# Kernel tuning notes

Hardware: AMD Instinct MI355X
Metric: run time of the kernel (lower is better)

The kernel has to match this reference:

```python
import jax, jax.numpy as jnp
import numpy as np

NUM_HEADS = 16
HEAD_DIM = 64
HIDDEN = NUM_HEADS * HEAD_DIM  # 1024
Q_DIM = 512
KV_DIM = 256


def setup_inputs() -> dict:
    key = jax.random.key(0)
    k1, k2, k3, k4, k5, k6 = jax.random.split(key, 6)
    B, I, J = 64, 128, 512  # num_assets, num_latents, window_size
    q = jax.random.normal(k1, (B, I, Q_DIM), dtype=jnp.float32)
    kv = jax.random.normal(k2, (B, J, KV_DIM), dtype=jnp.float32)
    # Linear weights stored as (in, out); fan-in scaled init
    Wq = jax.random.normal(k3, (Q_DIM, HIDDEN), dtype=jnp.float32) / np.sqrt(Q_DIM)
    Wkv = jax.random.normal(k4, (KV_DIM, 2 * HIDDEN), dtype=jnp.float32) / np.sqrt(KV_DIM)
    Wo = jax.random.normal(k5, (HIDDEN, Q_DIM), dtype=jnp.float32) / np.sqrt(HIDDEN)
    bo = jax.random.normal(k6, (Q_DIM,), dtype=jnp.float32) * 0.01
    return {"q": q, "kv": kv, "Wq": Wq, "Wkv": Wkv, "Wo": Wo, "bo": bo}


def reference(q, kv, Wq, Wkv, Wo, bo):
    B, I, _ = q.shape
    J = kv.shape[1]
    scale = HEAD_DIM ** -0.5
    query = q @ Wq                              # (B, I, HIDDEN)
    k, v = jnp.split(kv @ Wkv, 2, axis=-1)      # each (B, J, HIDDEN)
    qh = query.reshape(B, I, NUM_HEADS, HEAD_DIM).transpose(0, 2, 1, 3)  # bhid
    kh = k.reshape(B, J, NUM_HEADS, HEAD_DIM).transpose(0, 2, 1, 3)      # bhjd
    vh = v.reshape(B, J, NUM_HEADS, HEAD_DIM).transpose(0, 2, 1, 3)      # bhjd
    scores = jnp.einsum('bhid,bhjd->bhij', qh, kh) * scale
    attn = jax.nn.softmax(scores, axis=-1)
    out = jnp.einsum('bhij,bhjd->bhid', attn, vh)
    out = out.transpose(0, 2, 1, 3).reshape(B, I, HIDDEN)
    return out @ Wo + bo
```

## Files before the change

kernel.cpp:

```cpp
#include <hip/hip_runtime.h>
#include <stdint.h>

typedef unsigned short ushort_t;
typedef __attribute__((ext_vector_type(8))) short short8;
typedef __attribute__((ext_vector_type(4))) float floatx4;
typedef __attribute__((ext_vector_type(4))) float floatv4;
typedef __attribute__((ext_vector_type(4))) unsigned short ushortv4;


__device__ __forceinline__ ushort_t f2bf(float x) {
    union { float f; unsigned u; } v; v.f = x;
    unsigned r = v.u + 0x7fffu + ((v.u >> 16) & 1u);
    return (ushort_t)(r >> 16);
}

__device__ __forceinline__ void gl_lds16(const ushort_t* g, ushort_t* l) {
    __builtin_amdgcn_global_load_lds(
        (const __attribute__((address_space(1))) void*)g,
        (__attribute__((address_space(3))) void*)l, 16, 0, 0);
}

__global__ __launch_bounds__(256) void prep_kernel(
    const float* __restrict__ q, const float* __restrict__ kv,
    const float* __restrict__ Wq, const float* __restrict__ Wkv,
    const float* __restrict__ Wo,
    ushort_t* __restrict__ qA, ushort_t* __restrict__ kvA,
    ushort_t* __restrict__ WqT, ushort_t* __restrict__ WkvT,
    ushort_t* __restrict__ WoT)
{
    __shared__ ushort_t tileS[64 * 68];
    const int bid = blockIdx.x;
    const int tid = threadIdx.x;
    if (bid < 6144) {
        const float* src = (bid < 2048) ? q : kv;
        ushort_t* dst    = (bid < 2048) ? qA : kvA;
        size_t t = (size_t)(bid < 2048 ? bid : bid - 2048) * 256 + tid;
        const float* s = src + t * 8;
        floatv4 v0 = *(const floatv4*)s;
        floatv4 v1 = *(const floatv4*)(s + 4);
        short8 o;
        o[0] = (short)f2bf(v0[0]); o[1] = (short)f2bf(v0[1]);
        o[2] = (short)f2bf(v0[2]); o[3] = (short)f2bf(v0[3]);
        o[4] = (short)f2bf(v1[0]); o[5] = (short)f2bf(v1[1]);
        o[6] = (short)f2bf(v1[2]); o[7] = (short)f2bf(v1[3]);
        *(short8*)&dst[t * 8] = o;
        return;
    }
    const float* src; ushort_t* dst; int K, N, kt, nt; float scale = 1.0f;
    if (bid < 6272)      { int tl = bid - 6144; src = Wq;  dst = WqT;  K = 512;  N = 1024; kt = tl >> 4; nt = tl & 15; scale = 0.125f; }
    else if (bid < 6400) { int tl = bid - 6272; src = Wkv; dst = WkvT; K = 256;  N = 2048; kt = tl >> 5; nt = tl & 31; }
    else                 { int tl = bid - 6400; src = Wo;  dst = WoT;  K = 1024; N = 512;  kt = tl >> 3; nt = tl & 7;  }
#pragma unroll
    for (int t = 0; t < 4; t++) {
        int e = t * 256 + tid;
        int row = e >> 4, c4 = e & 15;
        floatv4 v = *(const floatv4*)&src[(size_t)(kt * 64 + row) * N + nt * 64 + c4 * 4];
        ushortv4 o;
        o[0] = f2bf(v[0] * scale); o[1] = f2bf(v[1] * scale);
        o[2] = f2bf(v[2] * scale); o[3] = f2bf(v[3] * scale);
        *(ushortv4*)&tileS[row * 68 + c4 * 4] = o;
    }
    __syncthreads();
#pragma unroll
    for (int t = 0; t < 4; t++) {
        int e = t * 256 + tid;
        int orow = e >> 4, c4 = e & 15;
        ushortv4 o;
#pragma unroll
        for (int e2 = 0; e2 < 4; e2++) o[e2] = tileS[(c4 * 4 + e2) * 68 + orow];
        *(ushortv4*)&dst[(size_t)(nt * 64 + orow) * K + kt * 64 + c4 * 4] = o;
    }
}

__global__ __launch_bounds__(256, 4) void gemm_bt_kernel(
    const ushort_t* __restrict__ A, const ushort_t* __restrict__ Bt,
    int M, int N, int K,
    float* __restrict__ out_f, const float* __restrict__ bias)
{
    __shared__ ushort_t smem[8192];
    ushort_t* sA = smem;
    ushort_t* sB = smem + 4096;

    const int bid  = blockIdx.x;
    const int xcd  = bid & 7;
    const int slot = bid >> 3;
    const int by   = xcd * 16 + (slot & 15);
    const int bx   = slot >> 4;

    const int tid  = threadIdx.x;
    const int lane = tid & 63;
    const int w    = tid >> 6;
    const int quad = lane >> 4;
    const int l15  = lane & 15;
    const int wr   = w >> 1, wc = w & 1;
    const int m0 = by * 64;
    const int n0 = bx * 64;

    const int rsub = lane >> 3;
    const int c8   = lane & 7;

    floatx4 acc[2][2];
#pragma unroll
    for (int i = 0; i < 2; i++)
#pragma unroll
        for (int j = 0; j < 2; j++) acc[i][j] = (floatx4){0.f, 0.f, 0.f, 0.f};

    for (int k0 = 0; k0 < K; k0 += 64) {
        __syncthreads();
#pragma unroll
        for (int t = 0; t < 2; t++) {
            int rg = w * 16 + t * 8;
            gl_lds16(&A[(size_t)(m0 + rg + rsub) * K + k0 + c8 * 8], &sA[rg * 64]);
            gl_lds16(&Bt[(size_t)(n0 + rg + rsub) * K + k0 + c8 * 8], &sB[rg * 64]);
        }
        __syncthreads();
#pragma unroll
        for (int ks = 0; ks < 64; ks += 32) {
            short8 af[2], bf[2];
#pragma unroll
            for (int i = 0; i < 2; i++)
                af[i] = *(const short8*)&sA[(wr * 32 + i * 16 + l15) * 64 + ks + quad * 8];
#pragma unroll
            for (int j = 0; j < 2; j++)
                bf[j] = *(const short8*)&sB[(wc * 32 + j * 16 + l15) * 64 + ks + quad * 8];
#pragma unroll
            for (int i = 0; i < 2; i++)
#pragma unroll
                for (int j = 0; j < 2; j++)
                    acc[i][j] = __builtin_amdgcn_mfma_f32_16x16x32_bf16(
                        af[i], bf[j], acc[i][j], 0, 0, 0);
        }
    }

#pragma unroll
    for (int i = 0; i < 2; i++)
#pragma unroll
        for (int j = 0; j < 2; j++)
#pragma unroll
            for (int r = 0; r < 4; r++) {
                int grow = m0 + wr * 32 + i * 16 + quad * 4 + r;
                int gcol = n0 + wc * 32 + j * 16 + l15;
                out_f[(size_t)grow * N + gcol] = acc[i][j][r] + bias[gcol];
            }
}

__global__ __launch_bounds__(512, 4) void fattn_kernel(
    const ushort_t* __restrict__ QA,
    const ushort_t* __restrict__ WQ,
    const ushort_t* __restrict__ KV,
    const ushort_t* __restrict__ W,
    ushort_t* __restrict__ O)
{
    __shared__ ushort_t smem[34816];
    ushort_t* sKV = smem;
    ushort_t* sKc = smem + 16384;
    ushort_t* sVt = smem + 20992;
    ushort_t* sP  = smem + 25600;
    ushort_t* sQ  = smem;
    ushort_t* sW  = smem + 16384;

    const int bid  = blockIdx.x;
    const int xcd  = bid & 7;
    const int slot = bid >> 3;
    const int b = xcd * 8 + (slot & 7);
    const int h = slot >> 3;

    const int tid  = threadIdx.x;
    const int lane = tid & 63, w = tid >> 6;
    const int quad = lane >> 4, l15 = lane & 15;
    const int swz  = (l15 & 7) << 3;

    ushort_t* sp = &sP[w * 1152];

    const int rq = lane >> 4;
    const int gq = l15 * 8;
    const int rh = lane >> 5;
    const int gk = (lane & 31) * 8;

    const ushort_t* qb = &QA[(size_t)b * 128 * 512];
    const ushort_t* wq = &WQ[(size_t)h * 64 * 512];
    floatx4 qacc[4];
#pragma unroll
    for (int nt = 0; nt < 4; nt++) qacc[nt] = (floatx4){0.f, 0.f, 0.f, 0.f};

    for (int kc = 0; kc < 4; kc++) {
        if (kc) __syncthreads();
#pragma unroll
        for (int t = 0; t < 4; t++) {
            int rb = w * 16 + t * 4;
            int srow = rb + rq;
            int scol = kc * 128 + (gq ^ ((srow & 7) << 3));
            gl_lds16(&qb[(size_t)srow * 512 + scol], &sQ[rb * 128]);
        }
#pragma unroll
        for (int t = 0; t < 2; t++) {
            int rb = w * 8 + t * 4;
            int srow = rb + rq;
            int scol = kc * 128 + (gq ^ ((srow & 7) << 3));
            gl_lds16(&wq[(size_t)srow * 512 + scol], &sW[rb * 128]);
        }
        __syncthreads();
#pragma unroll
        for (int ks = 0; ks < 4; ks++) {
            short8 af = *(const short8*)&sQ[(w * 16 + l15) * 128 + ((ks * 32 + quad * 8) ^ swz)];
#pragma unroll
            for (int nt = 0; nt < 4; nt++) {
                short8 bfr = *(const short8*)&sW[(nt * 16 + l15) * 128 + ((ks * 32 + quad * 8) ^ swz)];
                qacc[nt] = __builtin_amdgcn_mfma_f32_16x16x32_bf16(af, bfr, qacc[nt], 0, 0, 0);
            }
        }
    }
    __syncthreads();

    const ushort_t* kvb = &KV[(size_t)b * 512 * 256];
#define STAGE_KV(CH)                                                          \
    {                                                                         \
        _Pragma("unroll")                                                     \
        for (int t = 0; t < 4; t++) {                                         \
            int rloc = 8 * w + 2 * t;          \
            int srow = rloc + rh;                                             \
            int scol = gk ^ ((srow & 7) << 3);                                \
            gl_lds16(&kvb[(size_t)((CH) * 64 + srow) * 256 + scol],           \
                     &sKV[rloc * 256]);                                       \
        }                                                                     \
    }
    STAGE_KV(0);

#pragma unroll
    for (int nt = 0; nt < 4; nt++)
#pragma unroll
        for (int r = 0; r < 4; r++)
            sp[(quad * 4 + r) * 72 + nt * 16 + l15] = f2bf(qacc[nt][r]);
    short8 aq0 = *(const short8*)&sp[l15 * 72 + quad * 8];
    short8 aq1 = *(const short8*)&sp[l15 * 72 + 32 + quad * 8];

    short8 wf[8];
    {
        int n = w * 16 + l15;
        int grow = (n < 64) ? (h * 64 + n) : (1024 + h * 64 + (n - 64));
        const ushort_t* wp = &W[(size_t)grow * 256 + quad * 8];
#pragma unroll
        for (int ks = 0; ks < 8; ks++)
            wf[ks] = *(const short8*)(wp + ks * 32);
    }

    float lsum[4];
    floatx4 acc_o[4];
#pragma unroll
    for (int r = 0; r < 4; r++) lsum[r] = 0.f;
#pragma unroll
    for (int dt = 0; dt < 4; dt++) acc_o[dt] = (floatx4){0.f, 0.f, 0.f, 0.f};

    for (int ch = 0; ch < 8; ch++) {
        __syncthreads();

        floatx4 pacc[4];
#pragma unroll
        for (int jt = 0; jt < 4; jt++) pacc[jt] = (floatx4){0.f, 0.f, 0.f, 0.f};
#pragma unroll
        for (int ks = 0; ks < 8; ks++) {
            short8 af[4];
#pragma unroll
            for (int jt = 0; jt < 4; jt++)
                af[jt] = *(const short8*)&sKV[(jt * 16 + l15) * 256 + ((ks * 32 + quad * 8) ^ swz)];
#pragma unroll
            for (int jt = 0; jt < 4; jt++)
                pacc[jt] = __builtin_amdgcn_mfma_f32_16x16x32_bf16(
                    af[jt], wf[ks], pacc[jt], 0, 0, 0);
        }

        if (w < 4) {
            int d = w * 16 + l15;
#pragma unroll
            for (int jt = 0; jt < 4; jt++)
#pragma unroll
                for (int r = 0; r < 4; r++)
                    sKc[(jt * 16 + quad * 4 + r) * 72 + d] = f2bf(pacc[jt][r]);
        } else {
            int d = (w - 4) * 16 + l15;
#pragma unroll
            for (int jt = 0; jt < 4; jt++) {
                ushortv4 p;
#pragma unroll
                for (int r = 0; r < 4; r++) p[r] = f2bf(pacc[jt][r]);
                *(ushortv4*)&sVt[d * 72 + jt * 16 + quad * 4] = p;
            }
        }
        __syncthreads();

        if (ch < 7) STAGE_KV(ch + 1);

#pragma unroll
        for (int jt = 0; jt < 4; jt++) {
            const ushort_t* kp = &sKc[(jt * 16 + l15) * 72 + quad * 8];
            short8 bk0 = *(const short8*)kp;
            short8 bk1 = *(const short8*)(kp + 32);
            floatx4 a = (floatx4){0.f, 0.f, 0.f, 0.f};
            a = __builtin_amdgcn_mfma_f32_16x16x32_bf16(aq0, bk0, a, 0, 0, 0);
            a = __builtin_amdgcn_mfma_f32_16x16x32_bf16(aq1, bk1, a, 0, 0, 0);
            ushortv4 pk;
#pragma unroll
            for (int r = 0; r < 4; r++) {
                float p = __expf(a[r]);
                lsum[r] += p;
                pk[r] = f2bf(p);
            }
#pragma unroll
            for (int r = 0; r < 4; r++)
                sp[(quad * 4 + r) * 72 + jt * 16 + l15] = pk[r];
        }

#pragma unroll
        for (int kk = 0; kk < 2; kk++) {
            short8 ap = *(const short8*)&sp[l15 * 72 + kk * 32 + quad * 8];
#pragma unroll
            for (int dt = 0; dt < 4; dt++) {
                short8 bv = *(const short8*)&sVt[(dt * 16 + l15) * 72 + kk * 32 + quad * 8];
                acc_o[dt] = __builtin_amdgcn_mfma_f32_16x16x32_bf16(ap, bv, acc_o[dt], 0, 0, 0);
            }
        }
    }

#pragma unroll
    for (int r = 0; r < 4; r++) {
        float s = lsum[r];
#pragma unroll
        for (int off = 1; off < 16; off <<= 1) s += __shfl_xor(s, off);
        float inv = 1.0f / s;
        size_t rowo = (size_t)(b * 128 + w * 16 + quad * 4 + r) * 1024 + h * 64;
#pragma unroll
        for (int dt = 0; dt < 4; dt++)
            O[rowo + dt * 16 + l15] = f2bf(acc_o[dt][r] * inv);
    }
#undef STAGE_KV
}

extern "C" void kernel_launch(void* const* d_in, const int* in_sizes, int n_in,
                              void* d_out, int out_size, void* d_ws, size_t ws_size,
                              hipStream_t stream) {
    const float* q   = (const float*)d_in[0];
    const float* kv  = (const float*)d_in[1];
    const float* Wq  = (const float*)d_in[2];
    const float* Wkv = (const float*)d_in[3];
    const float* Wo  = (const float*)d_in[4];
    const float* bo  = (const float*)d_in[5];
    float* out = (float*)d_out;

    char* ws = (char*)d_ws;
    ushort_t* qA    = (ushort_t*)(ws + 0);
    ushort_t* kvA   = (ushort_t*)(ws + 8388608);
    ushort_t* WqT   = (ushort_t*)(ws + 25165824);
    ushort_t* WkvT  = (ushort_t*)(ws + 26214400);
    ushort_t* WoT   = (ushort_t*)(ws + 27262976);
    ushort_t* attnO = (ushort_t*)(ws + 45088768);

    hipLaunchKernelGGL(prep_kernel, dim3(6528), dim3(256), 0, stream,
                       q, kv, Wq, Wkv, Wo, qA, kvA, WqT, WkvT, WoT);

    hipLaunchKernelGGL(fattn_kernel, dim3(1024), dim3(512), 0, stream,
                       qA, WqT, kvA, WkvT, attnO);

    hipLaunchKernelGGL(gemm_bt_kernel, dim3(1024), dim3(256), 0, stream,
                       attnO, WoT, 8192, 512, 1024, out, bo);
}
```

Measured before the change: 202.4 us.

## Process two heads per attention block to share staged KV and Q tiles

The fused attention kernel now runs 1024-thread blocks covering two heads of the same batch item, halving the grid. Each block loads the KV chunk and the Q tile into LDS once and reuses them for both heads, with per-head K/V projection buffers. This cuts redundant global-to-LDS traffic for KV and Q. The cost is larger LDS use and bigger blocks, which may lower occupancy and make barriers more expensive.

```diff
diff --git a/kernel.cpp b/kernel.cpp
--- a/kernel.cpp
+++ b/kernel.cpp
@@ -144,33 +144,37 @@
             }
 }
 
-__global__ __launch_bounds__(512, 4) void fattn_kernel(
+__global__ __launch_bounds__(1024, 2) void fattn_kernel(
     const ushort_t* __restrict__ QA,
     const ushort_t* __restrict__ WQ,
     const ushort_t* __restrict__ KV,
     const ushort_t* __restrict__ W,
     ushort_t* __restrict__ O)
 {
-    __shared__ ushort_t smem[34816];
+    __shared__ ushort_t smem[53248];
     ushort_t* sKV = smem;
     ushort_t* sKc = smem + 16384;
-    ushort_t* sVt = smem + 20992;
-    ushort_t* sP  = smem + 25600;
+    ushort_t* sVt = smem + 25600;
+    ushort_t* sP  = smem + 34816;
     ushort_t* sQ  = smem;
     ushort_t* sW  = smem + 16384;
 
     const int bid  = blockIdx.x;
     const int xcd  = bid & 7;
     const int slot = bid >> 3;
-    const int b = xcd * 8 + (slot & 7);
-    const int h = slot >> 3;
+    const int b  = xcd * 8 + (slot & 7);
+    const int hp = slot >> 3;
 
     const int tid  = threadIdx.x;
     const int lane = tid & 63, w = tid >> 6;
+    const int hg   = w >> 3, wl = w & 7;
+    const int h    = hp * 2 + hg;
     const int quad = lane >> 4, l15 = lane & 15;
     const int swz  = (l15 & 7) << 3;
 
-    ushort_t* sp = &sP[w * 1152];
+    ushort_t* sp  = &sP[w * 1152];
+    ushort_t* sKc_g = &sKc[hg * 4608];
+    ushort_t* sVt_g = &sVt[hg * 4608];
 
     const int rq = lane >> 4;
     const int gq = l15 * 8;
@@ -178,34 +182,34 @@
     const int gk = (lane & 31) * 8;
 
     const ushort_t* qb = &QA[(size_t)b * 128 * 512];
-    const ushort_t* wq = &WQ[(size_t)h * 64 * 512];
+    const ushort_t* wqg = &WQ[(size_t)h * 64 * 512];
     floatx4 qacc[4];
 #pragma unroll
     for (int nt = 0; nt < 4; nt++) qacc[nt] = (floatx4){0.f, 0.f, 0.f, 0.f};
 
     for (int kc = 0; kc < 4; kc++) {
         if (kc) __syncthreads();
-#pragma unroll
-        for (int t = 0; t < 4; t++) {
-            int rb = w * 16 + t * 4;
-            int srow = rb + rq;
-            int scol = kc * 128 + (gq ^ ((srow & 7) << 3));
-            gl_lds16(&qb[(size_t)srow * 512 + scol], &sQ[rb * 128]);
-        }
 #pragma unroll
         for (int t = 0; t < 2; t++) {
             int rb = w * 8 + t * 4;
             int srow = rb + rq;
             int scol = kc * 128 + (gq ^ ((srow & 7) << 3));
-            gl_lds16(&wq[(size_t)srow * 512 + scol], &sW[rb * 128]);
+            gl_lds16(&qb[(size_t)srow * 512 + scol], &sQ[rb * 128]);
+        }
+#pragma unroll
+        for (int t = 0; t < 2; t++) {
+            int rb = wl * 8 + t * 4;
+            int srow = rb + rq;
+            int scol = kc * 128 + (gq ^ ((srow & 7) << 3));
+            gl_lds16(&wqg[(size_t)srow * 512 + scol], &sW[hg * 8192 + rb * 128]);
         }
         __syncthreads();
 #pragma unroll
         for (int ks = 0; ks < 4; ks++) {
-            short8 af = *(const short8*)&sQ[(w * 16 + l15) * 128 + ((ks * 32 + quad * 8) ^ swz)];
+            short8 af = *(const short8*)&sQ[(wl * 16 + l15) * 128 + ((ks * 32 + quad * 8) ^ swz)];
 #pragma unroll
             for (int nt = 0; nt < 4; nt++) {
-                short8 bfr = *(const short8*)&sW[(nt * 16 + l15) * 128 + ((ks * 32 + quad * 8) ^ swz)];
+                short8 bfr = *(const short8*)&sW[hg * 8192 + (nt * 16 + l15) * 128 + ((ks * 32 + quad * 8) ^ swz)];
                 qacc[nt] = __builtin_amdgcn_mfma_f32_16x16x32_bf16(af, bfr, qacc[nt], 0, 0, 0);
             }
         }
@@ -216,8 +220,8 @@
 #define STAGE_KV(CH)                                                          \
     {                                                                         \
         _Pragma("unroll")                                                     \
-        for (int t = 0; t < 4; t++) {                                         \
-            int rloc = 8 * w + 2 * t;          \
+        for (int t = 0; t < 2; t++) {                                         \
+            int rloc = 4 * w + 2 * t;          \
             int srow = rloc + rh;                                             \
             int scol = gk ^ ((srow & 7) << 3);                                \
             gl_lds16(&kvb[(size_t)((CH) * 64 + srow) * 256 + scol],           \
@@ -236,7 +240,7 @@
 
     short8 wf[8];
     {
-        int n = w * 16 + l15;
+        int n = wl * 16 + l15;
         int grow = (n < 64) ? (h * 64 + n) : (1024 + h * 64 + (n - 64));
         const ushort_t* wp = &W[(size_t)grow * 256 + quad * 8];
 #pragma unroll
@@ -269,21 +273,21 @@
                     af[jt], wf[ks], pacc[jt], 0, 0, 0);
         }
 
-        if (w < 4) {
-            int d = w * 16 + l15;
+        if (wl < 4) {
+            int d = wl * 16 + l15;
 #pragma unroll
             for (int jt = 0; jt < 4; jt++)
 #pragma unroll
                 for (int r = 0; r < 4; r++)
-                    sKc[(jt * 16 + quad * 4 + r) * 72 + d] = f2bf(pacc[jt][r]);
+                    sKc_g[(jt * 16 + quad * 4 + r) * 72 + d] = f2bf(pacc[jt][r]);
         } else {
-            int d = (w - 4) * 16 + l15;
+            int d = (wl - 4) * 16 + l15;
 #pragma unroll
             for (int jt = 0; jt < 4; jt++) {
                 ushortv4 p;
 #pragma unroll
                 for (int r = 0; r < 4; r++) p[r] = f2bf(pacc[jt][r]);
-                *(ushortv4*)&sVt[d * 72 + jt * 16 + quad * 4] = p;
+                *(ushortv4*)&sVt_g[d * 72 + jt * 16 + quad * 4] = p;
             }
         }
         __syncthreads();
@@ -292,7 +296,7 @@
 
 #pragma unroll
         for (int jt = 0; jt < 4; jt++) {
-            const ushort_t* kp = &sKc[(jt * 16 + l15) * 72 + quad * 8];
+            const ushort_t* kp = &sKc_g[(jt * 16 + l15) * 72 + quad * 8];
             short8 bk0 = *(const short8*)kp;
             short8 bk1 = *(const short8*)(kp + 32);
             floatx4 a = (floatx4){0.f, 0.f, 0.f, 0.f};
@@ -315,7 +319,7 @@
             short8 ap = *(const short8*)&sp[l15 * 72 + kk * 32 + quad * 8];
 #pragma unroll
             for (int dt = 0; dt < 4; dt++) {
-                short8 bv = *(const short8*)&sVt[(dt * 16 + l15) * 72 + kk * 32 + quad * 8];
+                short8 bv = *(const short8*)&sVt_g[(dt * 16 + l15) * 72 + kk * 32 + quad * 8];
                 acc_o[dt] = __builtin_amdgcn_mfma_f32_16x16x32_bf16(ap, bv, acc_o[dt], 0, 0, 0);
             }
         }
@@ -327,7 +331,7 @@
 #pragma unroll
         for (int off = 1; off < 16; off <<= 1) s += __shfl_xor(s, off);
         float inv = 1.0f / s;
-        size_t rowo = (size_t)(b * 128 + w * 16 + quad * 4 + r) * 1024 + h * 64;
+        size_t rowo = (size_t)(b * 128 + wl * 16 + quad * 4 + r) * 1024 + h * 64;
 #pragma unroll
         for (int dt = 0; dt < 4; dt++)
             O[rowo + dt * 16 + l15] = f2bf(acc_o[dt][r] * inv);
@@ -357,7 +361,7 @@
     hipLaunchKernelGGL(prep_kernel, dim3(6528), dim3(256), 0, stream,
                        q, kv, Wq, Wkv, Wo, qA, kvA, WqT, WkvT, WoT);
 
-    hipLaunchKernelGGL(fattn_kernel, dim3(1024), dim3(512), 0, stream,
+    hipLaunchKernelGGL(fattn_kernel, dim3(512), dim3(1024), 0, stream,
                        qA, WqT, kvA, WkvT, attnO);
 
     hipLaunchKernelGGL(gemm_bt_kernel, dim3(1024), dim3(256), 0, stream,
```

Result: slower. 212.9 us (+5.2%).
